# Kernel tuning notes

Measured on AMD Instinct MI355X. Metric: run time of the kernel, lower is better.

## Reference

```python
import jax, jax.numpy as jnp
import numpy as np

N_NODES = 100000
N_EDGES = 3200000  # avg degree 32
D_IN = 128
D_OUT = 64
BN_EPS = 0.001


def setup_inputs() -> dict:
    key = jax.random.key(0)
    k1, k2, k3, k4, k5 = jax.random.split(key, 5)
    x = jax.random.normal(k1, (N_NODES, D_IN), dtype=jnp.float32)
    W = jax.random.normal(k2, (D_IN, D_OUT), dtype=jnp.float32) * 0.05
    edge_val = jax.random.uniform(k3, (N_EDGES,), dtype=jnp.float32)
    edge_src = jax.random.randint(k4, (N_EDGES,), 0, N_NODES, dtype=jnp.int32)
    edge_dst = jax.random.randint(k5, (N_EDGES,), 0, N_NODES, dtype=jnp.int32)
    return {"x": x, "W": W, "edge_val": edge_val,
            "edge_src": edge_src, "edge_dst": edge_dst}


def reference(x, W, edge_val, edge_src, edge_dst):
    # pre_sup = X @ W  (dense feature transform; dropout rate is 0 -> identity)
    pre_sup = x @ W  # [N, D_OUT]
    # support = A @ pre_sup, A given in COO form: A[dst, src] = edge_val
    msgs = edge_val[:, None] * pre_sup[edge_src]          # [E, D_OUT]
    out = jax.ops.segment_sum(msgs, edge_dst, num_segments=N_NODES)  # [N, D_OUT]
    # tf.nn.moments over all-but-last axis + batch_norm (no scale/offset, eps=1e-3)
    mean = jnp.mean(out, axis=0)
    var = jnp.var(out, axis=0)
    out = (out - mean) * jax.lax.rsqrt(var + BN_EPS)
    return jax.nn.relu(out)
```

## Files before the change

### kernel.cpp

```cpp
#include <hip/hip_runtime.h>
#include <stdint.h>

#define D_IN  128
#define D_OUT 64
#define BN_EPS 1e-3f

#define BIN_SHIFT 6
#define BIN_NODES 64
#define BIN_CAP   2560
#define CHUNK     8192
#define MAX_BINS  1600

typedef __attribute__((ext_vector_type(8))) short bf16x8;
typedef __attribute__((ext_vector_type(4))) float f32x4;

__device__ __forceinline__ ushort f32_to_bf16_rne(float f) {
  uint u = __float_as_uint(f);
  u += 0x7FFFu + ((u >> 16) & 1u);
  return (ushort)(u >> 16);
}
__device__ __forceinline__ float bf16_to_f32(ushort h) {
  return __uint_as_float((uint)h << 16);
}

__global__ __launch_bounds__(256) void gemm_mfma_kernel(
    const float* __restrict__ x, const float* __restrict__ W,
    ushort* __restrict__ pre16, int n_nodes, int n_tiles) {
  __shared__ ushort Wb[D_IN * D_OUT];
  const int t = threadIdx.x;
  for (int i = t; i < D_IN * D_OUT; i += 256) Wb[i] = f32_to_bf16_rne(W[i]);
  __syncthreads();

  const int lane = t & 63;
  const int wave = t >> 6;
  const int m = lane & 15;
  const int quad = lane >> 4;

  bf16x8 bfrag[4][4];
#pragma unroll
  for (int nt = 0; nt < 4; ++nt)
#pragma unroll
    for (int s = 0; s < 4; ++s)
#pragma unroll
      for (int j = 0; j < 8; ++j)
        bfrag[nt][s][j] =
            (short)Wb[(32 * s + quad * 8 + j) * D_OUT + nt * 16 + m];

  for (int tile = blockIdx.x; tile < n_tiles; tile += gridDim.x) {
    const int rbase = tile * 64 + wave * 16;
    const int row = rbase + m;
    const size_t rl = (size_t)min(row, n_nodes - 1);
    f32x4 acc0 = {0.f, 0.f, 0.f, 0.f}, acc1 = {0.f, 0.f, 0.f, 0.f};
    f32x4 acc2 = {0.f, 0.f, 0.f, 0.f}, acc3 = {0.f, 0.f, 0.f, 0.f};
#pragma unroll
    for (int s = 0; s < 4; ++s) {
      const float4 xa = *(const float4*)&x[rl * D_IN + s * 32 + quad * 8];
      const float4 xb = *(const float4*)&x[rl * D_IN + s * 32 + quad * 8 + 4];
      bf16x8 af;
      af[0] = (short)f32_to_bf16_rne(xa.x);
      af[1] = (short)f32_to_bf16_rne(xa.y);
      af[2] = (short)f32_to_bf16_rne(xa.z);
      af[3] = (short)f32_to_bf16_rne(xa.w);
      af[4] = (short)f32_to_bf16_rne(xb.x);
      af[5] = (short)f32_to_bf16_rne(xb.y);
      af[6] = (short)f32_to_bf16_rne(xb.z);
      af[7] = (short)f32_to_bf16_rne(xb.w);
      acc0 = __builtin_amdgcn_mfma_f32_16x16x32_bf16(af, bfrag[0][s], acc0, 0, 0, 0);
      acc1 = __builtin_amdgcn_mfma_f32_16x16x32_bf16(af, bfrag[1][s], acc1, 0, 0, 0);
      acc2 = __builtin_amdgcn_mfma_f32_16x16x32_bf16(af, bfrag[2][s], acc2, 0, 0, 0);
      acc3 = __builtin_amdgcn_mfma_f32_16x16x32_bf16(af, bfrag[3][s], acc3, 0, 0, 0);
    }
#pragma unroll
    for (int reg = 0; reg < 4; ++reg) {
      const int r = rbase + quad * 4 + reg;
      if (r < n_nodes) {
        ushort* po = &pre16[(size_t)r * D_OUT + m];
        po[0]  = f32_to_bf16_rne(acc0[reg]);
        po[16] = f32_to_bf16_rne(acc1[reg]);
        po[32] = f32_to_bf16_rne(acc2[reg]);
        po[48] = f32_to_bf16_rne(acc3[reg]);
      }
    }
  }
}

__global__ __launch_bounds__(256) void partition_kernel(
    const float* __restrict__ ev, const int* __restrict__ esrc,
    const int* __restrict__ edst, int* __restrict__ bin_cursor,
    uint2* __restrict__ bucket, int n_edges, int n_bins) {
  __shared__ int cnt[MAX_BINS];
  __shared__ int base[MAX_BINS];
  const int t = threadIdx.x;
  const int beg = blockIdx.x * CHUNK;
  const int end = min(beg + CHUNK, n_edges);

  for (int i = t; i < n_bins; i += 256) cnt[i] = 0;
  __syncthreads();

  for (int i = beg + t * 4; i < end; i += 1024) {
    if (i + 3 < end) {
      const int4 d4 = *(const int4*)&edst[i];
      atomicAdd(&cnt[d4.x >> BIN_SHIFT], 1);
      atomicAdd(&cnt[d4.y >> BIN_SHIFT], 1);
      atomicAdd(&cnt[d4.z >> BIN_SHIFT], 1);
      atomicAdd(&cnt[d4.w >> BIN_SHIFT], 1);
    } else {
      for (int k = i; k < end; ++k) atomicAdd(&cnt[edst[k] >> BIN_SHIFT], 1);
    }
  }
  __syncthreads();

  for (int i = t; i < n_bins; i += 256) {
    const int c = cnt[i];
    int b = 0;
    if (c > 0) b = atomicAdd(&bin_cursor[i], c);
    if (b > BIN_CAP) b = BIN_CAP;
    base[i] = i * BIN_CAP + b;
    cnt[i] = 0;
  }
  __syncthreads();

  for (int i = beg + t * 4; i < end; i += 1024) {
    if (i + 3 < end) {
      const int4 d4 = *(const int4*)&edst[i];
      const int4 s4 = *(const int4*)&esrc[i];
      const float4 v4 = *(const float4*)&ev[i];
#pragma unroll
      for (int k = 0; k < 4; ++k) {
        const int dst = (&d4.x)[k];
        const int src = (&s4.x)[k];
        const float v = (&v4.x)[k];
        const int bin = dst >> BIN_SHIFT;
        const int r = atomicAdd(&cnt[bin], 1);
        const int pos = base[bin] + r;
        if (pos < (bin + 1) * BIN_CAP) {
          const uint w0 = ((uint)(dst & (BIN_NODES - 1)) << 17) | (uint)src;
          bucket[pos] = make_uint2(w0, __float_as_uint(v));
        }
      }
    } else {
      for (int k = i; k < end; ++k) {
        const int dst = edst[k];
        const int bin = dst >> BIN_SHIFT;
        const int r = atomicAdd(&cnt[bin], 1);
        const int pos = base[bin] + r;
        if (pos < (bin + 1) * BIN_CAP) {
          const uint w0 = ((uint)(dst & (BIN_NODES - 1)) << 17) | (uint)esrc[k];
          bucket[pos] = make_uint2(w0, __float_as_uint(ev[k]));
        }
      }
    }
  }
}

__global__ __launch_bounds__(256) void bin_sort_gather_kernel(
    const ushort* __restrict__ pre16, const uint2* __restrict__ bucket,
    const int* __restrict__ bin_cursor, float* __restrict__ out,
    float* __restrict__ stats, int n_nodes) {
  __shared__ uint s_src[BIN_CAP];
  __shared__ ushort s_val[BIN_CAP];
  __shared__ int s_hist[BIN_NODES];
  __shared__ int s_off[BIN_NODES + 1];
  __shared__ int s_cur[BIN_NODES];

  const int t = threadIdx.x;
  const int bin = blockIdx.x;
  const int cnt = min(bin_cursor[bin], BIN_CAP);
  const int64_t rbase = (int64_t)bin * BIN_CAP;

  if (t < BIN_NODES) s_hist[t] = 0;
  __syncthreads();

  for (int i = t; i < cnt; i += 256)
    atomicAdd(&s_hist[bucket[rbase + i].x >> 17], 1);
  __syncthreads();

  int own = (t < BIN_NODES) ? s_hist[t] : 0;
  for (int off = 1; off < BIN_NODES; off <<= 1) {
    int u = 0;
    if (t < BIN_NODES && t >= off) u = s_hist[t - off];
    __syncthreads();
    if (t < BIN_NODES) s_hist[t] += u;
    __syncthreads();
  }
  if (t < BIN_NODES) {
    const int e = s_hist[t] - own;
    s_off[t] = e;
    s_cur[t] = e;
  }
  if (t == 0) s_off[BIN_NODES] = cnt;
  __syncthreads();

  for (int i = t; i < cnt; i += 256) {
    const uint2 r = bucket[rbase + i];
    const int d = r.x >> 17;
    const int p = atomicAdd(&s_cur[d], 1);
    s_src[p] = r.x & 0x1FFFFu;
    s_val[p] = f32_to_bf16_rne(__uint_as_float(r.y));
  }
  __syncthreads();

  const int lane = t & 63;
  const int wave = t >> 6;
  const int half = lane >> 5;
  const int hl = lane & 31;
  const int node0 = bin * BIN_NODES;
  float csx = 0.f, csy = 0.f, cs2x = 0.f, cs2y = 0.f;

  for (int nl = wave; nl < BIN_NODES; nl += 4) {
    const int node = node0 + nl;
    if (node < n_nodes) {
      const int jb = s_off[nl], je = s_off[nl + 1];
      float a0x = 0.f, a0y = 0.f, a1x = 0.f, a1y = 0.f;
      float a2x = 0.f, a2y = 0.f, a3x = 0.f, a3y = 0.f;
      int j = jb + half;
      for (; j + 6 < je; j += 8) {
        const uint src0 = s_src[j],     src1 = s_src[j + 2];
        const uint src2 = s_src[j + 4], src3 = s_src[j + 6];
        const float v0 = bf16_to_f32(s_val[j]);
        const float v1 = bf16_to_f32(s_val[j + 2]);
        const float v2 = bf16_to_f32(s_val[j + 4]);
        const float v3 = bf16_to_f32(s_val[j + 6]);
        const uint p0 = *(const uint*)&pre16[(size_t)src0 * D_OUT + 2 * hl];
        const uint p1 = *(const uint*)&pre16[(size_t)src1 * D_OUT + 2 * hl];
        const uint p2 = *(const uint*)&pre16[(size_t)src2 * D_OUT + 2 * hl];
        const uint p3 = *(const uint*)&pre16[(size_t)src3 * D_OUT + 2 * hl];
        a0x += v0 * bf16_to_f32((ushort)(p0 & 0xFFFFu));
        a0y += v0 * bf16_to_f32((ushort)(p0 >> 16));
        a1x += v1 * bf16_to_f32((ushort)(p1 & 0xFFFFu));
        a1y += v1 * bf16_to_f32((ushort)(p1 >> 16));
        a2x += v2 * bf16_to_f32((ushort)(p2 & 0xFFFFu));
        a2y += v2 * bf16_to_f32((ushort)(p2 >> 16));
        a3x += v3 * bf16_to_f32((ushort)(p3 & 0xFFFFu));
        a3y += v3 * bf16_to_f32((ushort)(p3 >> 16));
      }
      for (; j < je; j += 2) {
        const uint src = s_src[j];
        const float v = bf16_to_f32(s_val[j]);
        const uint p = *(const uint*)&pre16[(size_t)src * D_OUT + 2 * hl];
        a0x += v * bf16_to_f32((ushort)(p & 0xFFFFu));
        a0y += v * bf16_to_f32((ushort)(p >> 16));
      }
      float ax = (a0x + a1x) + (a2x + a3x);
      float ay = (a0y + a1y) + (a2y + a3y);
      ax += __shfl_xor(ax, 32);
      ay += __shfl_xor(ay, 32);
      if (half == 0) {
        *(float2*)&out[(size_t)node * D_OUT + 2 * hl] = make_float2(ax, ay);
        csx += ax;
        cs2x += ax * ax;
        csy += ay;
        cs2y += ay * ay;
      }
    }
  }
  __syncthreads();

  float* red = (float*)s_src;
  float* red2 = red + 256;
  if (half == 0) {
    red[wave * 64 + 2 * hl] = csx;
    red[wave * 64 + 2 * hl + 1] = csy;
    red2[wave * 64 + 2 * hl] = cs2x;
    red2[wave * 64 + 2 * hl + 1] = cs2y;
  }
  __syncthreads();
  if (t < 64) {
    float s = red[t] + red[64 + t] + red[128 + t] + red[192 + t];
    float s2 = red2[t] + red2[64 + t] + red2[128 + t] + red2[192 + t];
    atomicAdd(&stats[t], s);
    atomicAdd(&stats[64 + t], s2);
  }
}

__global__ __launch_bounds__(256) void norm_kernel(
    float* __restrict__ out, const float* __restrict__ stats, int64_t n_vec4,
    float inv_n) {
  const int c = (threadIdx.x * 4) & 63;
  float mean[4], scale[4];
#pragma unroll
  for (int k = 0; k < 4; ++k) {
    mean[k] = stats[c + k] * inv_n;
    const float var = stats[64 + c + k] * inv_n - mean[k] * mean[k];
    scale[k] = rsqrtf(var + BN_EPS);
  }
  const int64_t stride = (int64_t)gridDim.x * 256;
  for (int64_t i = (int64_t)blockIdx.x * 256 + threadIdx.x; i < n_vec4;
       i += stride) {
    float4 v = ((float4*)out)[i];
    v.x = (v.x - mean[0]) * scale[0];
    v.y = (v.y - mean[1]) * scale[1];
    v.z = (v.z - mean[2]) * scale[2];
    v.w = (v.w - mean[3]) * scale[3];
    v.x = v.x > 0.f ? v.x : 0.f;
    v.y = v.y > 0.f ? v.y : 0.f;
    v.z = v.z > 0.f ? v.z : 0.f;
    v.w = v.w > 0.f ? v.w : 0.f;
    ((float4*)out)[i] = v;
  }
}

extern "C" void kernel_launch(void* const* d_in, const int* in_sizes, int n_in,
                              void* d_out, int out_size, void* d_ws,
                              size_t ws_size, hipStream_t stream) {
  const float* x = (const float*)d_in[0];
  const float* W = (const float*)d_in[1];
  const float* ev = (const float*)d_in[2];
  const int* esrc = (const int*)d_in[3];
  const int* edst = (const int*)d_in[4];

  const int n_nodes = in_sizes[0] / D_IN;
  const int n_edges = in_sizes[2];
  const int64_t n_out = (int64_t)n_nodes * D_OUT;
  const int n_bins = (n_nodes + BIN_NODES - 1) >> BIN_SHIFT;
  const int n_row_tiles = (n_nodes + 63) / 64;

  float* out = (float*)d_out;

  char* w = (char*)d_ws;
  ushort* pre16 = (ushort*)w;             w += (size_t)n_nodes * D_OUT * 2;
  int* bin_cursor = (int*)w;              w += (size_t)n_bins * 4;
  float* stats = (float*)w;               w += 128 * 4;
  w = (char*)(((uintptr_t)w + 7) & ~(uintptr_t)7);
  uint2* bucket = (uint2*)w;

  hipMemsetAsync(bin_cursor, 0, (size_t)n_bins * 4, stream);
  hipMemsetAsync(stats, 0, 128 * 4, stream);

  gemm_mfma_kernel<<<(n_row_tiles + 1) / 2, 256, 0, stream>>>(
      x, W, pre16, n_nodes, n_row_tiles);
  partition_kernel<<<(n_edges + CHUNK - 1) / CHUNK, 256, 0, stream>>>(
      ev, esrc, edst, bin_cursor, bucket, n_edges, n_bins);
  bin_sort_gather_kernel<<<n_bins, 256, 0, stream>>>(pre16, bucket, bin_cursor,
                                                     out, stats, n_nodes);
  norm_kernel<<<2048, 256, 0, stream>>>(out, stats, n_out / 4,
                                        1.0f / (float)n_nodes);
}
```

Before: 316.2 us.

## Split pre_sup into four 16-column slabs and gather per slab

The GEMM now writes pre_sup as four column slabs of 16 bf16 values each, so each node row in a slab is 32 bytes. The gather kernel launches four times as many blocks, one per (bin, slab) pair, and each wave covers 8 edges with 8 lanes per 32-byte row. The aim is a slab-sized working set small enough to stay in cache, making random gathers cheaper. In exchange the per-bin counting sort of bucket entries now runs four times, which adds bucket reads and LDS work, and the 32-byte gathers are narrower per edge.

```diff
diff --git a/kernel.cpp b/kernel.cpp
--- a/kernel.cpp
+++ b/kernel.cpp
@@ -45,6 +45,8 @@
       for (int j = 0; j < 8; ++j)
         bfrag[nt][s][j] =
             (short)Wb[(32 * s + quad * 8 + j) * D_OUT + nt * 16 + m];
+
+  const size_t slab = (size_t)n_nodes * 16;
 
   for (int tile = blockIdx.x; tile < n_tiles; tile += gridDim.x) {
     const int rbase = tile * 64 + wave * 16;
@@ -74,11 +76,11 @@
     for (int reg = 0; reg < 4; ++reg) {
       const int r = rbase + quad * 4 + reg;
       if (r < n_nodes) {
-        ushort* po = &pre16[(size_t)r * D_OUT + m];
-        po[0]  = f32_to_bf16_rne(acc0[reg]);
-        po[16] = f32_to_bf16_rne(acc1[reg]);
-        po[32] = f32_to_bf16_rne(acc2[reg]);
-        po[48] = f32_to_bf16_rne(acc3[reg]);
+        ushort* po = &pre16[(size_t)r * 16 + m];
+        po[0]        = f32_to_bf16_rne(acc0[reg]);
+        po[slab]     = f32_to_bf16_rne(acc1[reg]);
+        po[2 * slab] = f32_to_bf16_rne(acc2[reg]);
+        po[3 * slab] = f32_to_bf16_rne(acc3[reg]);
       }
     }
   }
@@ -156,7 +158,7 @@
 __global__ __launch_bounds__(256) void bin_sort_gather_kernel(
     const ushort* __restrict__ pre16, const uint2* __restrict__ bucket,
     const int* __restrict__ bin_cursor, float* __restrict__ out,
-    float* __restrict__ stats, int n_nodes) {
+    float* __restrict__ stats, int n_nodes, int n_bins) {
   __shared__ uint s_src[BIN_CAP];
   __shared__ ushort s_val[BIN_CAP];
   __shared__ int s_hist[BIN_NODES];
@@ -164,7 +166,8 @@
   __shared__ int s_cur[BIN_NODES];
 
   const int t = threadIdx.x;
-  const int bin = blockIdx.x;
+  const int bin = blockIdx.x % n_bins;
+  const int q = blockIdx.x / n_bins;
   const int cnt = min(bin_cursor[bin], BIN_CAP);
   const int64_t rbase = (int64_t)bin * BIN_CAP;
 
@@ -200,10 +203,11 @@
   }
   __syncthreads();
 
+  const ushort* __restrict__ slab = pre16 + (size_t)q * ((size_t)n_nodes * 16);
   const int lane = t & 63;
   const int wave = t >> 6;
-  const int half = lane >> 5;
-  const int hl = lane & 31;
+  const int rsel = lane >> 3;
+  const int c = lane & 7;
   const int node0 = bin * BIN_NODES;
   float csx = 0.f, csy = 0.f, cs2x = 0.f, cs2y = 0.f;
 
@@ -213,18 +217,19 @@
       const int jb = s_off[nl], je = s_off[nl + 1];
       float a0x = 0.f, a0y = 0.f, a1x = 0.f, a1y = 0.f;
       float a2x = 0.f, a2y = 0.f, a3x = 0.f, a3y = 0.f;
-      int j = jb + half;
-      for (; j + 6 < je; j += 8) {
-        const uint src0 = s_src[j],     src1 = s_src[j + 2];
-        const uint src2 = s_src[j + 4], src3 = s_src[j + 6];
-        const float v0 = bf16_to_f32(s_val[j]);
-        const float v1 = bf16_to_f32(s_val[j + 2]);
-        const float v2 = bf16_to_f32(s_val[j + 4]);
-        const float v3 = bf16_to_f32(s_val[j + 6]);
-        const uint p0 = *(const uint*)&pre16[(size_t)src0 * D_OUT + 2 * hl];
-        const uint p1 = *(const uint*)&pre16[(size_t)src1 * D_OUT + 2 * hl];
-        const uint p2 = *(const uint*)&pre16[(size_t)src2 * D_OUT + 2 * hl];
-        const uint p3 = *(const uint*)&pre16[(size_t)src3 * D_OUT + 2 * hl];
+      int base = jb;
+      for (; base + 32 <= je; base += 32) {
+        const int j0 = base + rsel;
+        const uint src0 = s_src[j0],      src1 = s_src[j0 + 8];
+        const uint src2 = s_src[j0 + 16], src3 = s_src[j0 + 24];
+        const float v0 = bf16_to_f32(s_val[j0]);
+        const float v1 = bf16_to_f32(s_val[j0 + 8]);
+        const float v2 = bf16_to_f32(s_val[j0 + 16]);
+        const float v3 = bf16_to_f32(s_val[j0 + 24]);
+        const uint p0 = *(const uint*)&slab[(size_t)src0 * 16 + 2 * c];
+        const uint p1 = *(const uint*)&slab[(size_t)src1 * 16 + 2 * c];
+        const uint p2 = *(const uint*)&slab[(size_t)src2 * 16 + 2 * c];
+        const uint p3 = *(const uint*)&slab[(size_t)src3 * 16 + 2 * c];
         a0x += v0 * bf16_to_f32((ushort)(p0 & 0xFFFFu));
         a0y += v0 * bf16_to_f32((ushort)(p0 >> 16));
         a1x += v1 * bf16_to_f32((ushort)(p1 & 0xFFFFu));
@@ -234,19 +239,27 @@
         a3x += v3 * bf16_to_f32((ushort)(p3 & 0xFFFFu));
         a3y += v3 * bf16_to_f32((ushort)(p3 >> 16));
       }
-      for (; j < je; j += 2) {
-        const uint src = s_src[j];
-        const float v = bf16_to_f32(s_val[j]);
-        const uint p = *(const uint*)&pre16[(size_t)src * D_OUT + 2 * hl];
-        a0x += v * bf16_to_f32((ushort)(p & 0xFFFFu));
-        a0y += v * bf16_to_f32((ushort)(p >> 16));
+      for (; base < je; base += 8) {
+        const int j = base + rsel;
+        if (j < je) {
+          const uint src = s_src[j];
+          const float v = bf16_to_f32(s_val[j]);
+          const uint p = *(const uint*)&slab[(size_t)src * 16 + 2 * c];
+          a0x += v * bf16_to_f32((ushort)(p & 0xFFFFu));
+          a0y += v * bf16_to_f32((ushort)(p >> 16));
+        }
       }
       float ax = (a0x + a1x) + (a2x + a3x);
       float ay = (a0y + a1y) + (a2y + a3y);
+      ax += __shfl_xor(ax, 8);
+      ax += __shfl_xor(ax, 16);
       ax += __shfl_xor(ax, 32);
+      ay += __shfl_xor(ay, 8);
+      ay += __shfl_xor(ay, 16);
       ay += __shfl_xor(ay, 32);
-      if (half == 0) {
-        *(float2*)&out[(size_t)node * D_OUT + 2 * hl] = make_float2(ax, ay);
+      if (rsel == 0) {
+        *(float2*)&out[(size_t)node * D_OUT + q * 16 + 2 * c] =
+            make_float2(ax, ay);
         csx += ax;
         cs2x += ax * ax;
         csy += ay;
@@ -257,19 +270,19 @@
   __syncthreads();
 
   float* red = (float*)s_src;
-  float* red2 = red + 256;
-  if (half == 0) {
-    red[wave * 64 + 2 * hl] = csx;
-    red[wave * 64 + 2 * hl + 1] = csy;
-    red2[wave * 64 + 2 * hl] = cs2x;
-    red2[wave * 64 + 2 * hl + 1] = cs2y;
-  }
-  __syncthreads();
-  if (t < 64) {
-    float s = red[t] + red[64 + t] + red[128 + t] + red[192 + t];
-    float s2 = red2[t] + red2[64 + t] + red2[128 + t] + red2[192 + t];
-    atomicAdd(&stats[t], s);
-    atomicAdd(&stats[64 + t], s2);
+  float* red2 = red + 64;
+  if (rsel == 0) {
+    red[wave * 16 + 2 * c] = csx;
+    red[wave * 16 + 2 * c + 1] = csy;
+    red2[wave * 16 + 2 * c] = cs2x;
+    red2[wave * 16 + 2 * c + 1] = cs2y;
+  }
+  __syncthreads();
+  if (t < 16) {
+    float s = red[t] + red[16 + t] + red[32 + t] + red[48 + t];
+    float s2 = red2[t] + red2[16 + t] + red2[32 + t] + red2[48 + t];
+    atomicAdd(&stats[q * 16 + t], s);
+    atomicAdd(&stats[64 + q * 16 + t], s2);
   }
 }
 
@@ -331,8 +344,8 @@
       x, W, pre16, n_nodes, n_row_tiles);
   partition_kernel<<<(n_edges + CHUNK - 1) / CHUNK, 256, 0, stream>>>(
       ev, esrc, edst, bin_cursor, bucket, n_edges, n_bins);
-  bin_sort_gather_kernel<<<n_bins, 256, 0, stream>>>(pre16, bucket, bin_cursor,
-                                                     out, stats, n_nodes);
+  bin_sort_gather_kernel<<<4 * n_bins, 256, 0, stream>>>(
+      pre16, bucket, bin_cursor, out, stats, n_nodes, n_bins);
   norm_kernel<<<2048, 256, 0, stream>>>(out, stats, n_out / 4,
                                         1.0f / (float)n_nodes);
 }
```

After: 381.4 us. +20.6%, slower.

## Sort bin edges by source quarter, stage GEMM output tiles, fold memsets into GEMM

Applied to the files above, without the earlier changes.

The gather kernel now sorts each bin's edges by (source-node quarter, destination) and walks the four source quarters in lockstep across all blocks, with barriers between phases. Per-node accumulators are held in registers across the phases. The aim is to concentrate concurrent gathers from pre16 into a smaller working set for better L2 locality. The GEMM stages its bf16 output tile through LDS so that global stores are coalesced 16-byte writes. It also zeroes bin_cursor and stats in block 0, replacing the two memset launches. Costs are more registers (32 accumulators per thread), a larger scan, and extra barriers.

```diff
diff --git a/kernel.cpp b/kernel.cpp
--- a/kernel.cpp
+++ b/kernel.cpp
@@ -10,6 +10,9 @@
 #define BIN_CAP   2560
 #define CHUNK     8192
 #define MAX_BINS  1600
+#define PT_STRIDE 72
+#define NQ    4
+#define NKEY  256
 
 typedef __attribute__((ext_vector_type(8))) short bf16x8;
 typedef __attribute__((ext_vector_type(4))) float f32x4;
@@ -25,9 +28,15 @@
 
 __global__ __launch_bounds__(256) void gemm_mfma_kernel(
     const float* __restrict__ x, const float* __restrict__ W,
-    ushort* __restrict__ pre16, int n_nodes, int n_tiles) {
+    ushort* __restrict__ pre16, int* __restrict__ bin_cursor,
+    float* __restrict__ stats, int n_bins, int n_nodes, int n_tiles) {
   __shared__ ushort Wb[D_IN * D_OUT];
+  __shared__ ushort ptile[64 * PT_STRIDE];
   const int t = threadIdx.x;
+  if (blockIdx.x == 0) {
+    for (int i = t; i < n_bins; i += 256) bin_cursor[i] = 0;
+    if (t < 128) stats[t] = 0.f;
+  }
   for (int i = t; i < D_IN * D_OUT; i += 256) Wb[i] = f32_to_bf16_rne(W[i]);
   __syncthreads();
 
@@ -47,8 +56,8 @@
             (short)Wb[(32 * s + quad * 8 + j) * D_OUT + nt * 16 + m];
 
   for (int tile = blockIdx.x; tile < n_tiles; tile += gridDim.x) {
-    const int rbase = tile * 64 + wave * 16;
-    const int row = rbase + m;
+    const int rbase0 = tile * 64;
+    const int row = rbase0 + wave * 16 + m;
     const size_t rl = (size_t)min(row, n_nodes - 1);
     f32x4 acc0 = {0.f, 0.f, 0.f, 0.f}, acc1 = {0.f, 0.f, 0.f, 0.f};
     f32x4 acc2 = {0.f, 0.f, 0.f, 0.f}, acc3 = {0.f, 0.f, 0.f, 0.f};
@@ -70,15 +79,25 @@
       acc2 = __builtin_amdgcn_mfma_f32_16x16x32_bf16(af, bfrag[2][s], acc2, 0, 0, 0);
       acc3 = __builtin_amdgcn_mfma_f32_16x16x32_bf16(af, bfrag[3][s], acc3, 0, 0, 0);
     }
+    __syncthreads();
 #pragma unroll
     for (int reg = 0; reg < 4; ++reg) {
-      const int r = rbase + quad * 4 + reg;
+      const int lr = wave * 16 + quad * 4 + reg;
+      ptile[lr * PT_STRIDE + m]      = f32_to_bf16_rne(acc0[reg]);
+      ptile[lr * PT_STRIDE + 16 + m] = f32_to_bf16_rne(acc1[reg]);
+      ptile[lr * PT_STRIDE + 32 + m] = f32_to_bf16_rne(acc2[reg]);
+      ptile[lr * PT_STRIDE + 48 + m] = f32_to_bf16_rne(acc3[reg]);
+    }
+    __syncthreads();
+    {
+      const int lr = t >> 2;
+      const int sg = t & 3;
+      const int r = rbase0 + lr;
       if (r < n_nodes) {
-        ushort* po = &pre16[(size_t)r * D_OUT + m];
-        po[0]  = f32_to_bf16_rne(acc0[reg]);
-        po[16] = f32_to_bf16_rne(acc1[reg]);
-        po[32] = f32_to_bf16_rne(acc2[reg]);
-        po[48] = f32_to_bf16_rne(acc3[reg]);
+        const uint4* pl = (const uint4*)&ptile[lr * PT_STRIDE + sg * 16];
+        uint4* po = (uint4*)&pre16[(size_t)r * D_OUT + sg * 16];
+        po[0] = pl[0];
+        po[1] = pl[1];
       }
     }
   }
@@ -156,46 +175,49 @@
 __global__ __launch_bounds__(256) void bin_sort_gather_kernel(
     const ushort* __restrict__ pre16, const uint2* __restrict__ bucket,
     const int* __restrict__ bin_cursor, float* __restrict__ out,
-    float* __restrict__ stats, int n_nodes) {
+    float* __restrict__ stats, int n_nodes, uint qmagic) {
   __shared__ uint s_src[BIN_CAP];
   __shared__ ushort s_val[BIN_CAP];
-  __shared__ int s_hist[BIN_NODES];
-  __shared__ int s_off[BIN_NODES + 1];
-  __shared__ int s_cur[BIN_NODES];
+  __shared__ int s_hist[NKEY];
+  __shared__ int s_off[NKEY + 1];
+  __shared__ int s_cur[NKEY];
+  __shared__ float red[4 * 64];
+  __shared__ float red2[4 * 64];
 
   const int t = threadIdx.x;
   const int bin = blockIdx.x;
   const int cnt = min(bin_cursor[bin], BIN_CAP);
   const int64_t rbase = (int64_t)bin * BIN_CAP;
 
-  if (t < BIN_NODES) s_hist[t] = 0;
-  __syncthreads();
-
-  for (int i = t; i < cnt; i += 256)
-    atomicAdd(&s_hist[bucket[rbase + i].x >> 17], 1);
-  __syncthreads();
-
-  int own = (t < BIN_NODES) ? s_hist[t] : 0;
-  for (int off = 1; off < BIN_NODES; off <<= 1) {
-    int u = 0;
-    if (t < BIN_NODES && t >= off) u = s_hist[t - off];
-    __syncthreads();
-    if (t < BIN_NODES) s_hist[t] += u;
-    __syncthreads();
-  }
-  if (t < BIN_NODES) {
-    const int e = s_hist[t] - own;
-    s_off[t] = e;
-    s_cur[t] = e;
-  }
-  if (t == 0) s_off[BIN_NODES] = cnt;
+  s_hist[t] = 0;
+  __syncthreads();
+
+  for (int i = t; i < cnt; i += 256) {
+    const uint w0 = bucket[rbase + i].x;
+    const uint src = w0 & 0x1FFFFu;
+    const uint q = (uint)(((uint64_t)src * qmagic) >> 35);
+    atomicAdd(&s_hist[(int)(q * BIN_NODES + (w0 >> 17))], 1);
+  }
+  __syncthreads();
+
+  const int own = s_hist[t];
+  for (int off = 1; off < NKEY; off <<= 1) {
+    const int u = (t >= off) ? s_hist[t - off] : 0;
+    __syncthreads();
+    s_hist[t] += u;
+    __syncthreads();
+  }
+  s_off[t] = s_hist[t] - own;
+  s_cur[t] = s_hist[t] - own;
+  if (t == 0) s_off[NKEY] = cnt;
   __syncthreads();
 
   for (int i = t; i < cnt; i += 256) {
     const uint2 r = bucket[rbase + i];
-    const int d = r.x >> 17;
-    const int p = atomicAdd(&s_cur[d], 1);
-    s_src[p] = r.x & 0x1FFFFu;
+    const uint src = r.x & 0x1FFFFu;
+    const uint q = (uint)(((uint64_t)src * qmagic) >> 35);
+    const int p = atomicAdd(&s_cur[(int)(q * BIN_NODES + (r.x >> 17))], 1);
+    s_src[p] = src;
     s_val[p] = f32_to_bf16_rne(__uint_as_float(r.y));
   }
   __syncthreads();
@@ -205,12 +227,17 @@
   const int half = lane >> 5;
   const int hl = lane & 31;
   const int node0 = bin * BIN_NODES;
-  float csx = 0.f, csy = 0.f, cs2x = 0.f, cs2y = 0.f;
-
-  for (int nl = wave; nl < BIN_NODES; nl += 4) {
-    const int node = node0 + nl;
-    if (node < n_nodes) {
-      const int jb = s_off[nl], je = s_off[nl + 1];
+
+  float accx[16], accy[16];
+#pragma unroll
+  for (int s = 0; s < 16; ++s) { accx[s] = 0.f; accy[s] = 0.f; }
+
+  for (int q = 0; q < NQ; ++q) {
+    const int kb = q * BIN_NODES;
+#pragma unroll
+    for (int s = 0; s < 16; ++s) {
+      const int nl = wave + s * 4;
+      const int jb = s_off[kb + nl], je = s_off[kb + nl + 1];
       float a0x = 0.f, a0y = 0.f, a1x = 0.f, a1y = 0.f;
       float a2x = 0.f, a2y = 0.f, a3x = 0.f, a3y = 0.f;
       int j = jb + half;
@@ -241,23 +268,27 @@
         a0x += v * bf16_to_f32((ushort)(p & 0xFFFFu));
         a0y += v * bf16_to_f32((ushort)(p >> 16));
       }
-      float ax = (a0x + a1x) + (a2x + a3x);
-      float ay = (a0y + a1y) + (a2y + a3y);
-      ax += __shfl_xor(ax, 32);
-      ay += __shfl_xor(ay, 32);
-      if (half == 0) {
-        *(float2*)&out[(size_t)node * D_OUT + 2 * hl] = make_float2(ax, ay);
-        csx += ax;
-        cs2x += ax * ax;
-        csy += ay;
-        cs2y += ay * ay;
-      }
-    }
-  }
-  __syncthreads();
-
-  float* red = (float*)s_src;
-  float* red2 = red + 256;
+      accx[s] += (a0x + a1x) + (a2x + a3x);
+      accy[s] += (a0y + a1y) + (a2y + a3y);
+    }
+    __syncthreads();
+  }
+
+  float csx = 0.f, csy = 0.f, cs2x = 0.f, cs2y = 0.f;
+#pragma unroll
+  for (int s = 0; s < 16; ++s) {
+    const int node = node0 + wave + s * 4;
+    float ax = accx[s], ay = accy[s];
+    ax += __shfl_xor(ax, 32);
+    ay += __shfl_xor(ay, 32);
+    if (half == 0 && node < n_nodes) {
+      *(float2*)&out[(size_t)node * D_OUT + 2 * hl] = make_float2(ax, ay);
+      csx += ax;
+      cs2x += ax * ax;
+      csy += ay;
+      cs2y += ay * ay;
+    }
+  }
   if (half == 0) {
     red[wave * 64 + 2 * hl] = csx;
     red[wave * 64 + 2 * hl + 1] = csy;
@@ -266,8 +297,8 @@
   }
   __syncthreads();
   if (t < 64) {
-    float s = red[t] + red[64 + t] + red[128 + t] + red[192 + t];
-    float s2 = red2[t] + red2[64 + t] + red2[128 + t] + red2[192 + t];
+    const float s = red[t] + red[64 + t] + red[128 + t] + red[192 + t];
+    const float s2 = red2[t] + red2[64 + t] + red2[128 + t] + red2[192 + t];
     atomicAdd(&stats[t], s);
     atomicAdd(&stats[64 + t], s2);
   }
@@ -315,6 +346,9 @@
   const int n_bins = (n_nodes + BIN_NODES - 1) >> BIN_SHIFT;
   const int n_row_tiles = (n_nodes + 63) / 64;
 
+  const uint q_size = (uint)((n_nodes + NQ - 1) / NQ);
+  const uint qmagic = (uint)(((1ull << 35) + q_size - 1) / q_size);
+
   float* out = (float*)d_out;
 
   char* w = (char*)d_ws;
@@ -324,15 +358,12 @@
   w = (char*)(((uintptr_t)w + 7) & ~(uintptr_t)7);
   uint2* bucket = (uint2*)w;
 
-  hipMemsetAsync(bin_cursor, 0, (size_t)n_bins * 4, stream);
-  hipMemsetAsync(stats, 0, 128 * 4, stream);
-
   gemm_mfma_kernel<<<(n_row_tiles + 1) / 2, 256, 0, stream>>>(
-      x, W, pre16, n_nodes, n_row_tiles);
+      x, W, pre16, bin_cursor, stats, n_bins, n_nodes, n_row_tiles);
   partition_kernel<<<(n_edges + CHUNK - 1) / CHUNK, 256, 0, stream>>>(
       ev, esrc, edst, bin_cursor, bucket, n_edges, n_bins);
-  bin_sort_gather_kernel<<<n_bins, 256, 0, stream>>>(pre16, bucket, bin_cursor,
-                                                     out, stats, n_nodes);
+  bin_sort_gather_kernel<<<n_bins, 256, 0, stream>>>(
+      pre16, bucket, bin_cursor, out, stats, n_nodes, qmagic);
   norm_kernel<<<2048, 256, 0, stream>>>(out, stats, n_out / 4,
                                         1.0f / (float)n_nodes);
 }
```

Result: slower. 489.3 us (+54.7%).
